# Kernel optimization log

Measured on AMD Instinct MI355X. Metric: run time of the kernel, lower is better.

Reference implementation:

```python
import jax, jax.numpy as jnp
import numpy as np

N, E, G = 50000, 800000, 512
C = 128          # in_channels = hidden_out_channel = out_channel
K = 3            # Chebyshev order (nb_filters)
NUM_EMB = 119    # largest OGB atom feature cardinality (padded common table)
EPS = 1e-5


def setup_inputs() -> dict:
    key = jax.random.key(0)
    ks = jax.random.split(key, 12)
    s = 0.05
    return {
        "atom_emb": jax.random.normal(ks[0], (9, NUM_EMB, C), jnp.float32) * s,
        "W1": jax.random.normal(ks[1], (K, C, C), jnp.float32) * s,
        "b1": jnp.zeros((C,), jnp.float32),
        "W3": jax.random.normal(ks[2], (K, C, C), jnp.float32) * s,
        "b3": jnp.zeros((C,), jnp.float32),
        "gamma": jnp.ones((C,), jnp.float32),
        "beta": jnp.zeros((C,), jnp.float32),
        "lw1": jax.random.normal(ks[3], (C, 16), jnp.float32) * s,
        "lb1": jnp.zeros((16,), jnp.float32),
        "lw2": jax.random.normal(ks[4], (16, 2), jnp.float32) * s,
        "lb2": jnp.zeros((2,), jnp.float32),
        "x": jax.random.randint(ks[5], (N, 9), 0, 2),
        "edge_index": jax.random.randint(ks[6], (2, E), 0, N),
        "batch": jnp.sort(jax.random.randint(ks[7], (N,), 0, G)),
    }


def _cheb_conv(h, row, col, norm, W, b):
    # PyG ChebConv, sym norm, lambda_max=2 => Lhat = -D^{-1/2} A D^{-1/2} (zero diag)
    def Lhat(z):
        return jax.ops.segment_sum(norm[:, None] * z[col], row, num_segments=N)
    Tx1 = Lhat(h)                      # T_1 = Lhat x
    Tx2 = 2.0 * Lhat(Tx1) - h          # T_2 = 2 Lhat T_1 - T_0
    return h @ W[0] + Tx1 @ W[1] + Tx2 @ W[2] + b


def reference(atom_emb, W1, b1, W3, b3, gamma, beta, lw1, lb1, lw2, lb2,
              x, edge_index, batch):
    row, col = edge_index[0], edge_index[1]
    # symmetric normalization weights (deg computed on row, as in get_laplacian)
    deg = jax.ops.segment_sum(jnp.ones((E,), jnp.float32), row, num_segments=N)
    dis = jnp.where(deg > 0, jax.lax.rsqrt(jnp.maximum(deg, 1.0)), 0.0)
    norm = -(dis[row] * dis[col])      # [E]

    # AtomEncoder: sum of 9 per-feature embeddings -> [N, C]
    h = atom_emb[jnp.arange(9), x].sum(axis=1)

    h = jax.nn.relu(_cheb_conv(h, row, col, norm, W1, b1))   # conv1
    h = jax.nn.relu(_cheb_conv(h, row, col, norm, W3, b3))   # conv3 (conv2 unused)

    # BatchNorm over nodes (training-mode batch stats, biased var)
    mu = h.mean(axis=0)
    var = jnp.mean((h - mu) ** 2, axis=0)
    h = (h - mu) * jax.lax.rsqrt(var + EPS) * gamma + beta

    # global_mean_pool over graphs
    sums = jax.ops.segment_sum(h, batch, num_segments=G)
    cnt = jax.ops.segment_sum(jnp.ones((N,), jnp.float32), batch, num_segments=G)
    pooled = sums / jnp.maximum(cnt, 1.0)[:, None]           # [G, C]

    out = jax.nn.relu(pooled @ lw1 + lb1) @ lw2 + lb2        # [G, 2]
    return out
```

## Files before the change

### kernel.cpp

```cpp
#include <hip/hip_runtime.h>
#include <hip/hip_bf16.h>

typedef __hip_bfloat16 bf16;
#define BN_EPS 1e-5f

typedef __attribute__((ext_vector_type(8))) short bf16x8;
typedef __attribute__((ext_vector_type(4))) float f32x4;

__device__ __forceinline__ float b2f(bf16 v){ return __bfloat162float(v); }
__device__ __forceinline__ float bu2f(unsigned short u){
  union { unsigned int i; float f; } x; x.i = ((unsigned int)u) << 16; return x.f;
}
__device__ __forceinline__ unsigned short f2bu(float f){
  bf16 b = __float2bfloat16(f);
  union { bf16 b; unsigned short u; } x; x.b = b; return x.u;
}
__device__ __forceinline__ float ldw(const void* p, size_t i, int wf){
  return wf ? ((const float*)p)[i] : b2f(((const bf16*)p)[i]);
}
__device__ __forceinline__ void up2(unsigned int w, float& lo, float& hi){
  union { unsigned int i; float f; } L, H;
  L.i = w << 16; H.i = w & 0xffff0000u;
  lo = L.f; hi = H.f;
}

__global__ void k_zero(int* __restrict__ p, int n,
                       const unsigned int* __restrict__ gbits, int* __restrict__ flag){
  int i = blockIdx.x * blockDim.x + threadIdx.x;
  if (i == 0) *flag = (gbits[0] == 0x3F800000u) ? 1 : 0;
  if (i < n) p[i] = 0;
}

__global__ void k_deg(const int* __restrict__ row, int E, int* __restrict__ rp){
  int e = blockIdx.x * blockDim.x + threadIdx.x;
  if (e < E) atomicAdd(&rp[row[e]], 1);
}

__global__ __launch_bounds__(256) void k_bsum(const int* __restrict__ rp, int N,
                                              int* __restrict__ bsum){
  int b = blockIdx.x;
  int base = b * 1024 + threadIdx.x * 4;
  int s = 0;
  #pragma unroll
  for (int j = 0; j < 4; ++j){ int i = base + j; if (i < N) s += rp[i]; }
  #pragma unroll
  for (int o = 32; o > 0; o >>= 1) s += __shfl_down(s, o);
  __shared__ int ws[4];
  int lane = threadIdx.x & 63, wv = threadIdx.x >> 6;
  if (lane == 0) ws[wv] = s;
  __syncthreads();
  if (threadIdx.x == 0) bsum[b] = ws[0] + ws[1] + ws[2] + ws[3];
}

__global__ __launch_bounds__(1024) void k_bscan(int* __restrict__ bsum, int B,
                                                int* __restrict__ rp, int N){
  __shared__ int ss[1024];
  int t = threadIdx.x;
  int v = (t < B) ? bsum[t] : 0;
  ss[t] = v; __syncthreads();
  for (int o = 1; o < 1024; o <<= 1){
    int u = (t >= o) ? ss[t - o] : 0;
    __syncthreads();
    ss[t] += u;
    __syncthreads();
  }
  if (t < B) bsum[t] = ss[t] - v;
  if (t == 1023) rp[N] = ss[1023];
}

__global__ __launch_bounds__(256) void k_scan3(int* __restrict__ rp, const int* __restrict__ bsum,
                                               int N, float* __restrict__ dis){
  int b = blockIdx.x;
  int t = threadIdx.x;
  int base = b * 1024 + t * 4;
  int d[4];
  #pragma unroll
  for (int j = 0; j < 4; ++j){ int i = base + j; d[j] = (i < N) ? rp[i] : 0; }
  int tsum = d[0] + d[1] + d[2] + d[3];
  __shared__ int ss[256];
  ss[t] = tsum; __syncthreads();
  for (int o = 1; o < 256; o <<= 1){
    int u = (t >= o) ? ss[t - o] : 0;
    __syncthreads();
    ss[t] += u;
    __syncthreads();
  }
  int run = bsum[b] + ss[t] - tsum;
  #pragma unroll
  for (int j = 0; j < 4; ++j){
    int i = base + j;
    if (i < N){
      rp[i] = run;
      run += d[j];
      dis[i] = (d[j] > 0) ? rsqrtf((float)d[j]) : 0.f;
    }
  }
}

__global__ __launch_bounds__(256) void k_prep(const int* __restrict__ rp, int N,
    int* __restrict__ gcur,
    const void* __restrict__ Wa, unsigned short* __restrict__ WTa,
    const void* __restrict__ Wb, unsigned short* __restrict__ WTb,
    const void* __restrict__ emb, const int* __restrict__ x, int NE,
    unsigned short* __restrict__ h, const int* __restrict__ flag){
  int b = blockIdx.x;
  int t = threadIdx.x;
  if (b == 0){
    int i = t << 8; if (i > N) i = N;
    gcur[t] = rp[i];
    return;
  }
  int wf = *flag;
  if (b <= 384){
    int id = (b - 1) * 256 + t;
    const void* W = (id < 49152) ? Wa : Wb;
    unsigned short* WT = (id < 49152) ? WTa : WTb;
    int i = (id < 49152) ? id : id - 49152;
    int r = i >> 7, n = i & 127;
    WT[(size_t)n * 384 + r] = f2bu(ldw(W, (size_t)r * 128 + n, wf));
    return;
  }
  int gid = (b - 385) * 256 + t;
  int n = gid >> 4, c8 = (gid & 15) << 3;
  if (n >= N) return;
  float s[8];
  #pragma unroll
  for (int j = 0; j < 8; ++j) s[j] = 0.f;
  #pragma unroll
  for (int f = 0; f < 9; ++f){
    int idx = x[n * 9 + f];
    size_t base = ((size_t)(f * NE + idx) << 7) + c8;
    if (wf){
      const float* ep = (const float*)emb + base;
      #pragma unroll
      for (int j = 0; j < 8; ++j) s[j] += ep[j];
    } else {
      uint4 v = *(const uint4*)((const unsigned short*)emb + base);
      float lo, hi;
      up2(v.x, lo, hi); s[0] += lo; s[1] += hi;
      up2(v.y, lo, hi); s[2] += lo; s[3] += hi;
      up2(v.z, lo, hi); s[4] += lo; s[5] += hi;
      up2(v.w, lo, hi); s[6] += lo; s[7] += hi;
    }
  }
  uint4 r;
  r.x = ((unsigned int)f2bu(s[1]) << 16) | f2bu(s[0]);
  r.y = ((unsigned int)f2bu(s[3]) << 16) | f2bu(s[2]);
  r.z = ((unsigned int)f2bu(s[5]) << 16) | f2bu(s[4]);
  r.w = ((unsigned int)f2bu(s[7]) << 16) | f2bu(s[6]);
  *(uint4*)(h + ((size_t)n << 7) + c8) = r;
}

__global__ __launch_bounds__(256) void k_bfill1(const int* __restrict__ row,
    const int* __restrict__ col, int E,
    int* __restrict__ gcur, unsigned int* __restrict__ ebuf){
  __shared__ int hist[256];
  __shared__ int curs[256];
  int t = threadIdx.x;
  hist[t] = 0;
  __syncthreads();
  int base = blockIdx.x * 4096;
  int r[16], c[16];
  #pragma unroll
  for (int j = 0; j < 16; ++j){
    int e = base + (j << 8) + t;
    if (e < E){
      r[j] = row[e]; c[j] = col[e];
      atomicAdd(&hist[r[j] >> 8], 1);
    } else r[j] = -1;
  }
  __syncthreads();
  int h = hist[t];
  if (h > 0) curs[t] = atomicAdd(&gcur[t], h);
  __syncthreads();
  #pragma unroll
  for (int j = 0; j < 16; ++j){
    if (r[j] >= 0){
      int p = atomicAdd(&curs[r[j] >> 8], 1);
      ebuf[p] = ((unsigned int)c[j] << 8) | ((unsigned int)r[j] & 255u);
    }
  }
}

__global__ __launch_bounds__(256) void k_bfill2(const unsigned int* __restrict__ ebuf,
    const int* __restrict__ rp, int N, const float* __restrict__ dis,
    int2* __restrict__ cpack){
  __shared__ int lcur[256];
  __shared__ float sdis[256];
  int b = blockIdx.x, t = threadIdx.x;
  int r0 = b << 8;
  int idx = r0 + t;
  int cl = idx < N ? idx : N;
  lcur[t] = rp[cl];
  sdis[t] = (idx < N) ? dis[idx] : 0.f;
  __syncthreads();
  int beg = rp[r0 < N ? r0 : N];
  int er = r0 + 256; if (er > N) er = N;
  int end = rp[er];
  for (int p = beg + t; p < end; p += 256){
    unsigned int pw = ebuf[p];
    int c = (int)(pw >> 8);
    int rl = (int)(pw & 255u);
    float nm = -(sdis[rl] * dis[c]);
    int slot = atomicAdd(&lcur[rl], 1);
    cpack[slot] = make_int2(c, __float_as_int(nm));
  }
}

__global__ __launch_bounds__(256) void k_spmm(const unsigned short* __restrict__ in,
    const int* __restrict__ rp, const int2* __restrict__ cpack,
    float alpha, const unsigned short* __restrict__ other, float beta,
    unsigned short* __restrict__ out, int N){
  int w = (blockIdx.x * 256 + threadIdx.x) >> 6;
  int lane = threadIdx.x & 63;
  if (w >= N) return;
  int half = lane >> 5, hl = lane & 31;
  int p0 = rp[w], p1 = rp[w + 1];
  float a0 = 0.f, a1 = 0.f, a2 = 0.f, a3 = 0.f;
  for (int p = p0; p < p1; p += 64){
    int m = p1 - p; if (m > 64) m = 64;
    int cj = 0; float nj = 0.f;
    if (lane < m){
      int2 pk = cpack[p + lane];
      cj = pk.x; nj = __int_as_float(pk.y);
    }
    for (int j = 0; j < m; j += 4){
      int e0 = j + half, e1 = j + 2 + half;
      int c0 = (e0 < m) ? __shfl(cj, e0) : -1;
      float w0 = __shfl(nj, e0);
      int c1 = (e1 < m) ? __shfl(cj, e1) : -1;
      float w1 = __shfl(nj, e1);
      if (c0 >= 0){
        ushort4 v = *(const ushort4*)(in + (((size_t)c0) << 7) + (hl << 2));
        a0 += w0 * bu2f(v.x); a1 += w0 * bu2f(v.y);
        a2 += w0 * bu2f(v.z); a3 += w0 * bu2f(v.w);
      }
      if (c1 >= 0){
        ushort4 v = *(const ushort4*)(in + (((size_t)c1) << 7) + (hl << 2));
        a0 += w1 * bu2f(v.x); a1 += w1 * bu2f(v.y);
        a2 += w1 * bu2f(v.z); a3 += w1 * bu2f(v.w);
      }
    }
  }
  a0 += __shfl_xor(a0, 32);
  a1 += __shfl_xor(a1, 32);
  a2 += __shfl_xor(a2, 32);
  a3 += __shfl_xor(a3, 32);
  if (half == 0){
    size_t o = (((size_t)w) << 7) + (hl << 2);
    a0 *= alpha; a1 *= alpha; a2 *= alpha; a3 *= alpha;
    if (other){
      ushort4 ov = *(const ushort4*)(other + o);
      a0 += beta * bu2f(ov.x); a1 += beta * bu2f(ov.y);
      a2 += beta * bu2f(ov.z); a3 += beta * bu2f(ov.w);
    }
    ushort4 r;
    r.x = f2bu(a0); r.y = f2bu(a1); r.z = f2bu(a2); r.w = f2bu(a3);
    *(ushort4*)(out + o) = r;
  }
}

__global__ __launch_bounds__(256) void k_conv(const unsigned short* __restrict__ X,
    const unsigned short* __restrict__ T1, const unsigned short* __restrict__ T2,
    const unsigned short* __restrict__ WT,
    const void* __restrict__ bias,
    unsigned short* __restrict__ Y, int N, const int* __restrict__ flag,
    float* __restrict__ bns){
  int wf = *flag;
  __shared__ unsigned short As[128 * 40];
  __shared__ unsigned short Ws[128 * 40];
  int t = threadIdx.x;
  int wv = t >> 6, lane = t & 63;
  int m16 = lane & 15, quad = lane >> 4;
  int n0 = blockIdx.x * 128;

  f32x4 acc[2][8];
  #pragma unroll
  for (int i = 0; i < 2; ++i)
    #pragma unroll
    for (int j = 0; j < 8; ++j) acc[i][j] = (f32x4){0.f, 0.f, 0.f, 0.f};

  for (int kc = 0; kc < 12; ++kc){
    const unsigned short* src = (kc < 4) ? X : ((kc < 8) ? T1 : T2);
    int koff = (kc & 3) << 5;
    int kg = kc << 5;
    #pragma unroll
    for (int i = 0; i < 2; ++i){
      int id = t + (i << 8);
      int r = id >> 2, ks = id & 3;
      int node = n0 + r;
      uint4 v = make_uint4(0, 0, 0, 0);
      if (node < N) v = *(const uint4*)(src + ((size_t)node << 7) + koff + (ks << 3));
      *(uint4*)((void*)(As + r * 40 + (ks << 3))) = v;
    }
    #pragma unroll
    for (int i = 0; i < 2; ++i){
      int id = t + (i << 8);
      int n = id >> 2, ks = id & 3;
      uint4 v = *(const uint4*)(WT + (size_t)n * 384 + kg + (ks << 3));
      *(uint4*)((void*)(Ws + n * 40 + (ks << 3))) = v;
    }
    __syncthreads();
    bf16x8 af[2];
    af[0] = *(const bf16x8*)((const void*)(As + (32 * wv + m16) * 40 + (quad << 3)));
    af[1] = *(const bf16x8*)((const void*)(As + (32 * wv + 16 + m16) * 40 + (quad << 3)));
    #pragma unroll
    for (int tn = 0; tn < 8; ++tn){
      bf16x8 bf_ = *(const bf16x8*)((const void*)(Ws + (16 * tn + m16) * 40 + (quad << 3)));
      acc[0][tn] = __builtin_amdgcn_mfma_f32_16x16x32_bf16(af[0], bf_, acc[0][tn], 0, 0, 0);
      acc[1][tn] = __builtin_amdgcn_mfma_f32_16x16x32_bf16(af[1], bf_, acc[1][tn], 0, 0, 0);
    }
    __syncthreads();
  }
  float bv[8];
  #pragma unroll
  for (int tn = 0; tn < 8; ++tn) bv[tn] = ldw(bias, 16 * tn + m16, wf);
  float ps[8], pq[8];
  #pragma unroll
  for (int tn = 0; tn < 8; ++tn){ ps[tn] = 0.f; pq[tn] = 0.f; }
  #pragma unroll
  for (int ri = 0; ri < 2; ++ri){
    #pragma unroll
    for (int r = 0; r < 4; ++r){
      int node = n0 + 32 * wv + 16 * ri + quad * 4 + r;
      if (node < N){
        #pragma unroll
        for (int tn = 0; tn < 8; ++tn){
          float v = fmaxf(acc[ri][tn][r] + bv[tn], 0.f);
          Y[((size_t)node << 7) + 16 * tn + m16] = f2bu(v);
          ps[tn] += v; pq[tn] += v * v;
        }
      }
    }
  }
  if (bns){
    float* redf = (float*)As;
    int rg = (wv << 2) | quad;
    #pragma unroll
    for (int tn = 0; tn < 8; ++tn) redf[rg * 128 + tn * 16 + m16] = ps[tn];
    __syncthreads();
    if (t < 128){
      float a = 0.f;
      #pragma unroll
      for (int r = 0; r < 16; ++r) a += redf[r * 128 + t];
      atomicAdd(&bns[t], a);
    }
    __syncthreads();
    #pragma unroll
    for (int tn = 0; tn < 8; ++tn) redf[rg * 128 + tn * 16 + m16] = pq[tn];
    __syncthreads();
    if (t < 128){
      float a = 0.f;
      #pragma unroll
      for (int r = 0; r < 16; ++r) a += redf[r * 128 + t];
      atomicAdd(&bns[128 + t], a);
    }
  }
}

__device__ __forceinline__ int lbound(const int* a, int n, int key){
  int lo = 0, hi = n;
  while (lo < hi){ int mid = (lo + hi) >> 1; if (a[mid] < key) lo = mid + 1; else hi = mid; }
  return lo;
}

__global__ __launch_bounds__(128) void k_pool(const unsigned short* __restrict__ h,
    const int* __restrict__ batchv, int N, const float* __restrict__ bns,
    const void* __restrict__ gamma, const void* __restrict__ beta,
    const void* __restrict__ lw1, const void* __restrict__ lb1,
    const void* __restrict__ lw2, const void* __restrict__ lb2,
    void* __restrict__ out, const int* __restrict__ flag){
  int wf = *flag;
  int g = blockIdx.x;
  int t = threadIdx.x;
  int c8 = (t & 15) << 3;
  int rg = t >> 4;
  __shared__ int slo, shi;
  if (t == 0){ slo = lbound(batchv, N, g); shi = lbound(batchv, N, g + 1); }
  __syncthreads();
  int lo = slo, hi = shi, cnt = hi - lo;
  float s[8];
  #pragma unroll
  for (int j = 0; j < 8; ++j) s[j] = 0.f;
  for (int n = lo + rg; n < hi; n += 8){
    uint4 v = *(const uint4*)(h + ((size_t)n << 7) + c8);
    float a, b;
    up2(v.x, a, b); s[0] += a; s[1] += b;
    up2(v.y, a, b); s[2] += a; s[3] += b;
    up2(v.z, a, b); s[4] += a; s[5] += b;
    up2(v.w, a, b); s[6] += a; s[7] += b;
  }
  __shared__ float red[8][128];
  *(float4*)(&red[rg][c8])     = (float4){s[0], s[1], s[2], s[3]};
  *(float4*)(&red[rg][c8 + 4]) = (float4){s[4], s[5], s[6], s[7]};
  __syncthreads();
  int c = t;
  float acc = 0.f;
  #pragma unroll
  for (int r = 0; r < 8; ++r) acc += red[r][c];
  float pooled = acc / (float)(cnt > 0 ? cnt : 1);
  float mu = bns[c] / (float)N;
  float var = bns[128 + c] / (float)N - mu * mu;
  float sc = ldw(gamma, c, wf) * rsqrtf(var + BN_EPS);
  float sh = ldw(beta, c, wf) - mu * sc;
  float pb = (cnt > 0) ? (pooled * sc + sh) : 0.f;
  __shared__ float sp[128];
  __shared__ float hid[16];
  sp[c] = pb; __syncthreads();
  if (c < 16){
    float sm = ldw(lb1, c, wf);
    for (int i = 0; i < 128; ++i) sm += sp[i] * ldw(lw1, i * 16 + c, wf);
    hid[c] = fmaxf(sm, 0.f);
  }
  __syncthreads();
  if (c < 2){
    float sm = ldw(lb2, c, wf);
    for (int j = 0; j < 16; ++j) sm += hid[j] * ldw(lw2, j * 2 + c, wf);
    if (wf) ((float*)out)[g * 2 + c] = sm;
    else    ((bf16*)out)[g * 2 + c] = __float2bfloat16(sm);
  }
}

extern "C" void kernel_launch(void* const* d_in, const int* in_sizes, int n_in,
                              void* d_out, int out_size, void* d_ws, size_t ws_size,
                              hipStream_t stream){
  const void* emb   = d_in[0];
  const void* W1    = d_in[1];
  const void* b1    = d_in[2];
  const void* W3    = d_in[3];
  const void* b3    = d_in[4];
  const void* gamma = d_in[5];
  const void* beta  = d_in[6];
  const void* lw1   = d_in[7];
  const void* lb1   = d_in[8];
  const void* lw2   = d_in[9];
  const void* lb2   = d_in[10];
  const int* x      = (const int*)d_in[11];
  const int* ei     = (const int*)d_in[12];
  const int* batchv = (const int*)d_in[13];
  (void)n_in; (void)ws_size;

  int N  = in_sizes[13];
  int E  = in_sizes[12] / 2;
  int NE = in_sizes[0] / (9 * 128);
  int G  = out_size / 2;
  const int* row = ei;
  const int* col = ei + E;

  char* ws = (char*)d_ws;
  size_t off = 0;
  auto alloc = [&](size_t bytes) -> char* {
    char* p = ws + off;
    off += (bytes + 255) & ~(size_t)255;
    return p;
  };
  int*   flag = (int*)alloc(4);
  int*   rp   = (int*)alloc((size_t)(N + 1) * 4);
  float* bns  = (float*)alloc(256 * 4);
  size_t zero_end = off;
  float* dis  = (float*)alloc((size_t)N * 4);
  int*   bsum = (int*)alloc(1024 * 4);
  int*   gcur = (int*)alloc(256 * 4);
  unsigned int* ebuf = (unsigned int*)alloc((size_t)E * 4);
  int2*  cpack = (int2*)alloc((size_t)E * 8);
  unsigned short* wt1 = (unsigned short*)alloc(49152 * 2);
  unsigned short* wt2 = (unsigned short*)alloc(49152 * 2);
  size_t fb = ((size_t)N * 128 * 2 + 255) & ~(size_t)255;
  unsigned short* Hf = (unsigned short*)alloc(fb);
  unsigned short* Tf = (unsigned short*)alloc(fb);
  unsigned short* Zf = (unsigned short*)alloc(fb);

  int zints = (int)((zero_end - 256) / 4);
  k_zero<<<(zints + 255) / 256, 256, 0, stream>>>(rp, zints, (const unsigned int*)gamma, flag);

  int eb = (E + 255) / 256;
  int B  = (N + 1023) / 1024;
  int NB = (N + 255) / 256;
  k_deg  <<<eb, 256, 0, stream>>>(row, E, rp);
  k_bsum <<<B, 256, 0, stream>>>(rp, N, bsum);
  k_bscan<<<1, 1024, 0, stream>>>(bsum, B, rp, N);
  k_scan3<<<B, 256, 0, stream>>>(rp, bsum, N, dis);
  int pb = 385 + (int)(((size_t)N * 16 + 255) / 256);
  k_prep<<<pb, 256, 0, stream>>>(rp, N, gcur, W1, wt1, W3, wt2, emb, x, NE, Hf, flag);
  k_bfill1<<<(E + 4095) / 4096, 256, 0, stream>>>(row, col, E, gcur, ebuf);
  k_bfill2<<<NB, 256, 0, stream>>>(ebuf, rp, N, dis, cpack);

  int sb = (N + 3) / 4;
  int cb = (N + 127) / 128;
  k_spmm<<<sb, 256, 0, stream>>>(Hf, rp, cpack, 1.f, nullptr, 0.f, Tf, N);
  k_spmm<<<sb, 256, 0, stream>>>(Tf, rp, cpack, 2.f, Hf, -1.f, Zf, N);
  k_conv<<<cb, 256, 0, stream>>>(Hf, Tf, Zf, wt1, b1, Hf, N, flag, nullptr);
  k_spmm<<<sb, 256, 0, stream>>>(Hf, rp, cpack, 1.f, nullptr, 0.f, Tf, N);
  k_spmm<<<sb, 256, 0, stream>>>(Tf, rp, cpack, 2.f, Hf, -1.f, Zf, N);
  k_conv<<<cb, 256, 0, stream>>>(Hf, Tf, Zf, wt2, b3, Hf, N, flag, bns);

  k_pool<<<G, 128, 0, stream>>>(Hf, batchv, N, bns, gamma, beta, lw1, lb1, lw2, lb2,
                                d_out, flag);
}
```

Measured before the change: 383.9 us.

## Build CSR via bucket histogram instead of global degree atomics and scans

Replaces the per-edge global degree atomics and the three-kernel multi-block prefix scan with a per-block shared-memory histogram over 256-row buckets, a single-block bucket scan, and a per-bucket local count and scan that produces row pointers and degree normalisation. The aim is to remove 800k scattered global atomics and several small scan launches from CSR construction. In exchange it adds a second pass over the bucketed edge buffer, and the buckets are assumed to number at most 256, so N is limited to about 65k nodes.

```diff
diff --git a/kernel.cpp b/kernel.cpp
--- a/kernel.cpp
+++ b/kernel.cpp
@@ -31,88 +31,51 @@
   if (i < n) p[i] = 0;
 }
 
-__global__ void k_deg(const int* __restrict__ row, int E, int* __restrict__ rp){
-  int e = blockIdx.x * blockDim.x + threadIdx.x;
-  if (e < E) atomicAdd(&rp[row[e]], 1);
-}
-
-__global__ __launch_bounds__(256) void k_bsum(const int* __restrict__ rp, int N,
-                                              int* __restrict__ bsum){
-  int b = blockIdx.x;
-  int base = b * 1024 + threadIdx.x * 4;
-  int s = 0;
-  #pragma unroll
-  for (int j = 0; j < 4; ++j){ int i = base + j; if (i < N) s += rp[i]; }
-  #pragma unroll
-  for (int o = 32; o > 0; o >>= 1) s += __shfl_down(s, o);
-  __shared__ int ws[4];
-  int lane = threadIdx.x & 63, wv = threadIdx.x >> 6;
-  if (lane == 0) ws[wv] = s;
-  __syncthreads();
-  if (threadIdx.x == 0) bsum[b] = ws[0] + ws[1] + ws[2] + ws[3];
-}
-
-__global__ __launch_bounds__(1024) void k_bscan(int* __restrict__ bsum, int B,
-                                                int* __restrict__ rp, int N){
-  __shared__ int ss[1024];
-  int t = threadIdx.x;
-  int v = (t < B) ? bsum[t] : 0;
+__global__ __launch_bounds__(256) void k_bhist(const int* __restrict__ row, int E,
+                                               int* __restrict__ gcnt){
+  __shared__ int hist[256];
+  int t = threadIdx.x;
+  hist[t] = 0;
+  __syncthreads();
+  int base = blockIdx.x * 4096;
+  #pragma unroll
+  for (int j = 0; j < 16; ++j){
+    int e = base + (j << 8) + t;
+    if (e < E) atomicAdd(&hist[row[e] >> 8], 1);
+  }
+  __syncthreads();
+  int h = hist[t];
+  if (h > 0) atomicAdd(&gcnt[t], h);
+}
+
+__global__ __launch_bounds__(256) void k_bbase(const int* __restrict__ gcnt,
+    int* __restrict__ bucketBase, int* __restrict__ gcur, int* __restrict__ rp, int N){
+  __shared__ int ss[256];
+  int t = threadIdx.x;
+  int v = gcnt[t];
   ss[t] = v; __syncthreads();
-  for (int o = 1; o < 1024; o <<= 1){
-    int u = (t >= o) ? ss[t - o] : 0;
-    __syncthreads();
-    ss[t] += u;
-    __syncthreads();
-  }
-  if (t < B) bsum[t] = ss[t] - v;
-  if (t == 1023) rp[N] = ss[1023];
-}
-
-__global__ __launch_bounds__(256) void k_scan3(int* __restrict__ rp, const int* __restrict__ bsum,
-                                               int N, float* __restrict__ dis){
-  int b = blockIdx.x;
-  int t = threadIdx.x;
-  int base = b * 1024 + t * 4;
-  int d[4];
-  #pragma unroll
-  for (int j = 0; j < 4; ++j){ int i = base + j; d[j] = (i < N) ? rp[i] : 0; }
-  int tsum = d[0] + d[1] + d[2] + d[3];
-  __shared__ int ss[256];
-  ss[t] = tsum; __syncthreads();
   for (int o = 1; o < 256; o <<= 1){
     int u = (t >= o) ? ss[t - o] : 0;
     __syncthreads();
     ss[t] += u;
     __syncthreads();
   }
-  int run = bsum[b] + ss[t] - tsum;
-  #pragma unroll
-  for (int j = 0; j < 4; ++j){
-    int i = base + j;
-    if (i < N){
-      rp[i] = run;
-      run += d[j];
-      dis[i] = (d[j] > 0) ? rsqrtf((float)d[j]) : 0.f;
-    }
-  }
-}
-
-__global__ __launch_bounds__(256) void k_prep(const int* __restrict__ rp, int N,
-    int* __restrict__ gcur,
+  int ex = ss[t] - v;
+  bucketBase[t] = ex;
+  gcur[t] = ex;
+  if (t == 255){ bucketBase[256] = ss[255]; rp[N] = ss[255]; }
+}
+
+__global__ __launch_bounds__(256) void k_prep(int N,
     const void* __restrict__ Wa, unsigned short* __restrict__ WTa,
     const void* __restrict__ Wb, unsigned short* __restrict__ WTb,
     const void* __restrict__ emb, const int* __restrict__ x, int NE,
     unsigned short* __restrict__ h, const int* __restrict__ flag){
   int b = blockIdx.x;
   int t = threadIdx.x;
-  if (b == 0){
-    int i = t << 8; if (i > N) i = N;
-    gcur[t] = rp[i];
-    return;
-  }
   int wf = *flag;
-  if (b <= 384){
-    int id = (b - 1) * 256 + t;
+  if (b < 384){
+    int id = b * 256 + t;
     const void* W = (id < 49152) ? Wa : Wb;
     unsigned short* WT = (id < 49152) ? WTa : WTb;
     int i = (id < 49152) ? id : id - 49152;
@@ -120,7 +83,7 @@
     WT[(size_t)n * 384 + r] = f2bu(ldw(W, (size_t)r * 128 + n, wf));
     return;
   }
-  int gid = (b - 385) * 256 + t;
+  int gid = (b - 384) * 256 + t;
   int n = gid >> 4, c8 = (gid & 15) << 3;
   if (n >= N) return;
   float s[8];
@@ -182,21 +145,44 @@
   }
 }
 
-__global__ __launch_bounds__(256) void k_bfill2(const unsigned int* __restrict__ ebuf,
-    const int* __restrict__ rp, int N, const float* __restrict__ dis,
-    int2* __restrict__ cpack){
+__global__ __launch_bounds__(256) void k_bfill2a(const unsigned int* __restrict__ ebuf,
+    const int* __restrict__ bucketBase, int N,
+    int* __restrict__ rp, float* __restrict__ dis){
+  __shared__ int cnt[256];
+  __shared__ int ss[256];
+  int b = blockIdx.x, t = threadIdx.x;
+  cnt[t] = 0;
+  __syncthreads();
+  int beg = bucketBase[b], end = bucketBase[b + 1];
+  for (int p = beg + t; p < end; p += 256)
+    atomicAdd(&cnt[ebuf[p] & 255u], 1);
+  __syncthreads();
+  int v = cnt[t];
+  ss[t] = v; __syncthreads();
+  for (int o = 1; o < 256; o <<= 1){
+    int u = (t >= o) ? ss[t - o] : 0;
+    __syncthreads();
+    ss[t] += u;
+    __syncthreads();
+  }
+  int idx = (b << 8) + t;
+  if (idx < N){
+    rp[idx] = beg + ss[t] - v;
+    dis[idx] = (v > 0) ? rsqrtf((float)v) : 0.f;
+  }
+}
+
+__global__ __launch_bounds__(256) void k_bfill2b(const unsigned int* __restrict__ ebuf,
+    const int* __restrict__ bucketBase, const int* __restrict__ rp, int N,
+    const float* __restrict__ dis, int2* __restrict__ cpack){
   __shared__ int lcur[256];
   __shared__ float sdis[256];
   int b = blockIdx.x, t = threadIdx.x;
-  int r0 = b << 8;
-  int idx = r0 + t;
-  int cl = idx < N ? idx : N;
-  lcur[t] = rp[cl];
+  int idx = (b << 8) + t;
+  lcur[t] = (idx < N) ? rp[idx] : 0;
   sdis[t] = (idx < N) ? dis[idx] : 0.f;
   __syncthreads();
-  int beg = rp[r0 < N ? r0 : N];
-  int er = r0 + 256; if (er > N) er = N;
-  int end = rp[er];
+  int beg = bucketBase[b], end = bucketBase[b + 1];
   for (int p = beg + t; p < end; p += 256){
     unsigned int pw = ebuf[p];
     int c = (int)(pw >> 8);
@@ -455,12 +441,12 @@
     return p;
   };
   int*   flag = (int*)alloc(4);
+  int*   gcnt = (int*)alloc(256 * 4);
+  float* bns  = (float*)alloc(256 * 4);
+  int*   bucketBase = (int*)alloc(257 * 4);
+  int*   gcur = (int*)alloc(256 * 4);
   int*   rp   = (int*)alloc((size_t)(N + 1) * 4);
-  float* bns  = (float*)alloc(256 * 4);
-  size_t zero_end = off;
   float* dis  = (float*)alloc((size_t)N * 4);
-  int*   bsum = (int*)alloc(1024 * 4);
-  int*   gcur = (int*)alloc(256 * 4);
   unsigned int* ebuf = (unsigned int*)alloc((size_t)E * 4);
   int2*  cpack = (int2*)alloc((size_t)E * 8);
   unsigned short* wt1 = (unsigned short*)alloc(49152 * 2);
@@ -470,20 +456,17 @@
   unsigned short* Tf = (unsigned short*)alloc(fb);
   unsigned short* Zf = (unsigned short*)alloc(fb);
 
-  int zints = (int)((zero_end - 256) / 4);
-  k_zero<<<(zints + 255) / 256, 256, 0, stream>>>(rp, zints, (const unsigned int*)gamma, flag);
-
-  int eb = (E + 255) / 256;
-  int B  = (N + 1023) / 1024;
-  int NB = (N + 255) / 256;
-  k_deg  <<<eb, 256, 0, stream>>>(row, E, rp);
-  k_bsum <<<B, 256, 0, stream>>>(rp, N, bsum);
-  k_bscan<<<1, 1024, 0, stream>>>(bsum, B, rp, N);
-  k_scan3<<<B, 256, 0, stream>>>(rp, bsum, N, dis);
-  int pb = 385 + (int)(((size_t)N * 16 + 255) / 256);
-  k_prep<<<pb, 256, 0, stream>>>(rp, N, gcur, W1, wt1, W3, wt2, emb, x, NE, Hf, flag);
-  k_bfill1<<<(E + 4095) / 4096, 256, 0, stream>>>(row, col, E, gcur, ebuf);
-  k_bfill2<<<NB, 256, 0, stream>>>(ebuf, rp, N, dis, cpack);
+  k_zero<<<2, 256, 0, stream>>>(gcnt, 512, (const unsigned int*)gamma, flag);
+
+  int ebk = (E + 4095) / 4096;
+  int NB  = (N + 255) / 256;
+  k_bhist<<<ebk, 256, 0, stream>>>(row, E, gcnt);
+  k_bbase<<<1, 256, 0, stream>>>(gcnt, bucketBase, gcur, rp, N);
+  int pb = 384 + (int)(((size_t)N * 16 + 255) / 256);
+  k_prep<<<pb, 256, 0, stream>>>(N, W1, wt1, W3, wt2, emb, x, NE, Hf, flag);
+  k_bfill1<<<ebk, 256, 0, stream>>>(row, col, E, gcur, ebuf);
+  k_bfill2a<<<NB, 256, 0, stream>>>(ebuf, bucketBase, N, rp, dis);
+  k_bfill2b<<<NB, 256, 0, stream>>>(ebuf, bucketBase, rp, N, dis, cpack);
 
   int sb = (N + 3) / 4;
   int cb = (N + 127) / 128;
```

Result: faster. 353.5 us (median of 2 runs) (-7.9%).
